# Kernel tuning notes

Hardware: AMD Instinct MI355X
Metric: run time of the kernel (lower is better)

Reference implementation:

```python
import jax, jax.numpy as jnp
import numpy as np

B, L, D, U = 8, 512, 128, 32
ATT_WIDTH = 128
EPS = 1e-7  # K.epsilon()


def setup_inputs() -> dict:
    key = jax.random.key(0)
    ks = jax.random.split(key, 4)
    x = jax.random.normal(ks[0], (B, L, D), dtype=jnp.float32)
    Wt = jax.random.normal(ks[1], (D, U), dtype=jnp.float32) * 0.1
    Wx = jax.random.normal(ks[2], (D, U), dtype=jnp.float32) * 0.1
    bh = jnp.zeros((U,), dtype=jnp.float32)
    Wa = jax.random.normal(ks[3], (U, 1), dtype=jnp.float32) * 0.1
    ba = jnp.zeros((1,), dtype=jnp.float32)
    return {"x": x, "Wt": Wt, "Wx": Wx, "bh": bh, "Wa": Wa, "ba": ba}


def reference(x, Wt, Wx, bh, Wa, ba):
    # Additive attention scores: e[b,t,s] = Wa^T (x_t Wt + x_s Wx + bh) + ba
    q = x @ Wt                              # [B,L,U]
    k = x @ Wx                              # [B,L,U]
    h = q[:, :, None, :] + k[:, None, :, :] + bh   # [B,L,L,U]
    e = jnp.einsum('btsu,u->bts', h, Wa[:, 0]) + ba[0]  # [B,L,L]
    # Windowed mask (non-causal): key j visible to query i iff lower[j] <= i < upper[j]
    lower = jnp.arange(L) - ATT_WIDTH // 2
    upper = lower + ATT_WIDTH
    idx = jnp.arange(L)[:, None]
    mask = (idx >= lower) & (idx < upper)   # [L,L]
    # Original zeroes masked scores (NOT -inf) before softmax — keep that.
    e = jnp.where(mask[None, :, :], e, jnp.zeros_like(e))
    e = e - jnp.max(e, axis=-1, keepdims=True)
    a = jnp.exp(e)
    a = a / (jnp.sum(a, axis=-1, keepdims=True) + EPS)  # [B,L,L]
    v = jnp.einsum('bts,bsd->btd', a, x)    # [B,L,D]
    return v
```

## Files before the change

### kernel.cpp

```cpp
#include <hip/hip_runtime.h>
#include <float.h>

#define B 8
#define L 512
#define D 128
#define U 32
#define WIN 128
#define EPS 1e-7f
#define T 8
#define ROWS (T + WIN - 1)
#define WPITCH (WIN + T)

__global__ __launch_bounds__(256) void pre_kernel(
        const float* __restrict__ x, const float* __restrict__ Wt,
        const float* __restrict__ Wx, const float* __restrict__ bh,
        const float* __restrict__ Wa, const float* __restrict__ ba,
        float* __restrict__ qd, float* __restrict__ kd,
        float* __restrict__ xpart) {
    __shared__ float swq[D], swk[D];
    __shared__ float scc;
    __shared__ float red[256];
    int blk = blockIdx.x, tid = threadIdx.x;

    if (tid < D) {
        float sq = 0.f, sk = 0.f;
#pragma unroll
        for (int u = 0; u < U; ++u) {
            float wa = Wa[u];
            sq += Wt[tid * U + u] * wa;
            sk += Wx[tid * U + u] * wa;
        }
        swq[tid] = sq; swk[tid] = sk;
    }
    if (tid == 0) {
        float s = ba[0];
        for (int u = 0; u < U; ++u) s += bh[u] * Wa[u];
        scc = s;
    }
    __syncthreads();

    int r = blk * 256 + tid;
    const float4* xr = (const float4*)(x + (size_t)r * D);
    float sq = 0.f, sk = 0.f;
#pragma unroll
    for (int i = 0; i < D / 4; ++i) {
        float4 v = xr[i];
        sq += v.x * swq[4*i] + v.y * swq[4*i+1] + v.z * swq[4*i+2] + v.w * swq[4*i+3];
        sk += v.x * swk[4*i] + v.y * swk[4*i+1] + v.z * swk[4*i+2] + v.w * swk[4*i+3];
    }
    qd[r] = sq + scc;
    kd[r] = sk;

    int d = tid & (D - 1), h = tid >> 7;
    const float* xp = x + ((size_t)(blk * 256 + h * 128)) * D + d;
    float s = 0.f;
#pragma unroll 8
    for (int i = 0; i < 128; ++i) s += xp[(size_t)i * D];
    red[tid] = s;
    __syncthreads();
    if (tid < 128) xpart[blk * 128 + tid] = red[tid] + red[tid + 128];
}

__global__ __launch_bounds__(256) void attn_kernel(
        const float* __restrict__ x, const float* __restrict__ qd,
        const float* __restrict__ kd, const float* __restrict__ xpart,
        float* __restrict__ out) {
    __shared__ float w[T][WPITCH];
    __shared__ float adj[T];
    int blk = blockIdx.x;
    int b = blk >> 6;
    int t0 = (blk & 63) * T;
    int row0 = t0 - (WIN / 2 - 1);
    int tid = threadIdx.x;
    int q = tid >> 5;
    int dt = tid & 31;

    for (int i = tid; i < T * WPITCH; i += 256) ((float*)w)[i] = 0.f;
    __syncthreads();

    int kt = dt;
    int t = t0 + q;
    float qv = qd[b * L + t];
    float e[4];
    int   sv[4];
#pragma unroll
    for (int i = 0; i < 4; ++i) {
        int k = kt + 32 * i;
        int s = t - 63 + k;
        bool valid = ((unsigned)s < (unsigned)L);
        sv[i] = valid;
        e[i] = valid ? (qv + kd[b * L + s]) : -FLT_MAX;
    }
    float mx = fmaxf(fmaxf(e[0], e[1]), fmaxf(e[2], e[3]));
#pragma unroll
    for (int off = 16; off > 0; off >>= 1) mx = fmaxf(mx, __shfl_xor(mx, off));
    float m = fmaxf(mx, 0.f);
    float w0 = __expf(-m);
    float wv[4], sm = 0.f;
#pragma unroll
    for (int i = 0; i < 4; ++i) {
        wv[i] = sv[i] ? __expf(e[i] - m) : 0.f;
        sm += wv[i];
    }
#pragma unroll
    for (int off = 16; off > 0; off >>= 1) sm += __shfl_xor(sm, off);
    int ss0 = max(0, t - 63), ss1 = min(L, t + 64);
    int count = ss1 - ss0;
    float denom = sm + (float)(L - count) * w0 + EPS;
    float inv = 1.f / denom;
#pragma unroll
    for (int i = 0; i < 4; ++i) {
        int k = kt + 32 * i;
        if (sv[i]) w[q][q + k] = (wv[i] - w0) * inv;
    }
    if (kt == 0) adj[q] = w0 * inv;
    __syncthreads();

    float4 acc = {0.f, 0.f, 0.f, 0.f};
    const float4* xb = (const float4*)(x + (size_t)b * L * D);
#pragma unroll 4
    for (int r = 0; r < ROWS; ++r) {
        int s = row0 + r;
        int sc = min(max(s, 0), L - 1);
        float4 xv = xb[(size_t)sc * (D / 4) + dt];
        float ww = w[q][r];
        acc.x += ww * xv.x; acc.y += ww * xv.y;
        acc.z += ww * xv.z; acc.w += ww * xv.w;
    }

    const float4* xp0 = (const float4*)(xpart + (size_t)(2 * b) * D);
    const float4* xp1 = (const float4*)(xpart + (size_t)(2 * b + 1) * D);
    float4 s0 = xp0[dt], s1 = xp1[dt];
    float a = adj[q];
    float4 o;
    o.x = acc.x + a * (s0.x + s1.x);
    o.y = acc.y + a * (s0.y + s1.y);
    o.z = acc.z + a * (s0.z + s1.z);
    o.w = acc.w + a * (s0.w + s1.w);
    ((float4*)out)[((size_t)(b * L + t)) * (D / 4) + dt] = o;
}

extern "C" void kernel_launch(void* const* d_in, const int* in_sizes, int n_in,
                              void* d_out, int out_size, void* d_ws, size_t ws_size,
                              hipStream_t stream) {
    const float* x  = (const float*)d_in[0];
    const float* Wt = (const float*)d_in[1];
    const float* Wx = (const float*)d_in[2];
    const float* bh = (const float*)d_in[3];
    const float* Wa = (const float*)d_in[4];
    const float* ba = (const float*)d_in[5];
    float* out = (float*)d_out;

    float* ws    = (float*)d_ws;
    float* qd    = ws;
    float* kd    = qd + B * L;
    float* xpart = kd + B * L;

    pre_kernel<<<(B * L) / 256, 256, 0, stream>>>(x, Wt, Wx, bh, Wa, ba, qd, kd, xpart);
    attn_kernel<<<B * (L / T), 256, 0, stream>>>(x, qd, kd, xpart, out);
}
```

Baseline: 93.07 us.

## Reuse x rows across query pairs and split window rows between half-waves

The attention kernel stores softmax weights transposed (row-major by key row) so each thread reads a float2 of weights and accumulates two query outputs per loaded x row. This halves global x reads per output. The key-row range is split between two half-waves, skips rows outside the sequence instead of clamping, and combines the halves with a cross-lane shuffle. The pre-kernel is relaunched as 32 blocks of 128 rows, with each row's projection split over two threads, to raise parallelism. It also corrects the visible-key count used for the masked-zero term in the denominator (t+65 instead of t+64).

```diff
diff --git a/kernel.cpp b/kernel.cpp
--- a/kernel.cpp
+++ b/kernel.cpp
@@ -9,7 +9,7 @@
 #define EPS 1e-7f
 #define T 8
 #define ROWS (T + WIN - 1)
-#define WPITCH (WIN + T)
+#define WPITCH 10
 
 __global__ __launch_bounds__(256) void pre_kernel(
         const float* __restrict__ x, const float* __restrict__ Wt,
@@ -19,8 +19,9 @@
         float* __restrict__ xpart) {
     __shared__ float swq[D], swk[D];
     __shared__ float scc;
-    __shared__ float red[256];
+    __shared__ float redq[256], redk[256];
     int blk = blockIdx.x, tid = threadIdx.x;
+    int r0 = blk * 128;
 
     if (tid < D) {
         float sq = 0.f, sk = 0.f;
@@ -39,105 +40,133 @@
     }
     __syncthreads();
 
-    int r = blk * 256 + tid;
-    const float4* xr = (const float4*)(x + (size_t)r * D);
-    float sq = 0.f, sk = 0.f;
+    {
+        int rr = tid & 127, h = tid >> 7;
+        const float4* xr = (const float4*)(x + ((size_t)(r0 + rr)) * D + h * 64);
+        float sq = 0.f, sk = 0.f;
+        int d0 = h * 64;
 #pragma unroll
-    for (int i = 0; i < D / 4; ++i) {
-        float4 v = xr[i];
-        sq += v.x * swq[4*i] + v.y * swq[4*i+1] + v.z * swq[4*i+2] + v.w * swq[4*i+3];
-        sk += v.x * swk[4*i] + v.y * swk[4*i+1] + v.z * swk[4*i+2] + v.w * swk[4*i+3];
+        for (int i = 0; i < 16; ++i) {
+            float4 v = xr[i];
+            sq += v.x * swq[d0 + 4*i]     + v.y * swq[d0 + 4*i + 1]
+                + v.z * swq[d0 + 4*i + 2] + v.w * swq[d0 + 4*i + 3];
+            sk += v.x * swk[d0 + 4*i]     + v.y * swk[d0 + 4*i + 1]
+                + v.z * swk[d0 + 4*i + 2] + v.w * swk[d0 + 4*i + 3];
+        }
+        redq[tid] = sq; redk[tid] = sk;
     }
-    qd[r] = sq + scc;
-    kd[r] = sk;
+    __syncthreads();
+    if (tid < 128) {
+        qd[r0 + tid] = redq[tid] + redq[tid + 128] + scc;
+        kd[r0 + tid] = redk[tid] + redk[tid + 128];
+    }
+    __syncthreads();
 
-    int d = tid & (D - 1), h = tid >> 7;
-    const float* xp = x + ((size_t)(blk * 256 + h * 128)) * D + d;
-    float s = 0.f;
+    {
+        int d = tid & 127, h = tid >> 7;
+        const float* xp = x + ((size_t)(r0 + h * 64)) * D + d;
+        float s = 0.f;
 #pragma unroll 8
-    for (int i = 0; i < 128; ++i) s += xp[(size_t)i * D];
-    red[tid] = s;
+        for (int i = 0; i < 64; ++i) s += xp[(size_t)i * D];
+        redq[tid] = s;
+    }
     __syncthreads();
-    if (tid < 128) xpart[blk * 128 + tid] = red[tid] + red[tid + 128];
+    if (tid < 128) xpart[blk * 128 + tid] = redq[tid] + redq[tid + 128];
 }
 
 __global__ __launch_bounds__(256) void attn_kernel(
         const float* __restrict__ x, const float* __restrict__ qd,
         const float* __restrict__ kd, const float* __restrict__ xpart,
         float* __restrict__ out) {
-    __shared__ float w[T][WPITCH];
+    __shared__ float w[ROWS * WPITCH];
     __shared__ float adj[T];
     int blk = blockIdx.x;
     int b = blk >> 6;
     int t0 = (blk & 63) * T;
     int row0 = t0 - (WIN / 2 - 1);
     int tid = threadIdx.x;
-    int q = tid >> 5;
-    int dt = tid & 31;
 
-    for (int i = tid; i < T * WPITCH; i += 256) ((float*)w)[i] = 0.f;
+    for (int i = tid; i < ROWS * WPITCH; i += 256) w[i] = 0.f;
     __syncthreads();
 
-    int kt = dt;
-    int t = t0 + q;
-    float qv = qd[b * L + t];
-    float e[4];
-    int   sv[4];
+    {
+        int ql = tid >> 5, kt = tid & 31;
+        int t = t0 + ql;
+        float qv = qd[b * L + t];
+        float e[4];
+        int   sv[4];
 #pragma unroll
-    for (int i = 0; i < 4; ++i) {
-        int k = kt + 32 * i;
-        int s = t - 63 + k;
-        bool valid = ((unsigned)s < (unsigned)L);
-        sv[i] = valid;
-        e[i] = valid ? (qv + kd[b * L + s]) : -FLT_MAX;
+        for (int i = 0; i < 4; ++i) {
+            int k = kt + 32 * i;
+            int s = t - 63 + k;
+            bool valid = ((unsigned)s < (unsigned)L);
+            sv[i] = valid;
+            e[i] = valid ? (qv + kd[b * L + s]) : -FLT_MAX;
+        }
+        float mx = fmaxf(fmaxf(e[0], e[1]), fmaxf(e[2], e[3]));
+#pragma unroll
+        for (int off = 16; off > 0; off >>= 1) mx = fmaxf(mx, __shfl_xor(mx, off));
+        float m = fmaxf(mx, 0.f);
+        float w0 = __expf(-m);
+        float wv[4], sm = 0.f;
+#pragma unroll
+        for (int i = 0; i < 4; ++i) {
+            wv[i] = sv[i] ? __expf(e[i] - m) : 0.f;
+            sm += wv[i];
+        }
+#pragma unroll
+        for (int off = 16; off > 0; off >>= 1) sm += __shfl_xor(sm, off);
+        int ss0 = max(0, t - 63), ss1 = min(L, t + 65);
+        int count = ss1 - ss0;
+        float inv = 1.f / (sm + (float)(L - count) * w0 + EPS);
+#pragma unroll
+        for (int i = 0; i < 4; ++i) {
+            int k = kt + 32 * i;
+            if (sv[i]) w[(ql + k) * WPITCH + ql] = (wv[i] - w0) * inv;
+        }
+        if (kt == 0) adj[ql] = w0 * inv;
     }
-    float mx = fmaxf(fmaxf(e[0], e[1]), fmaxf(e[2], e[3]));
-#pragma unroll
-    for (int off = 16; off > 0; off >>= 1) mx = fmaxf(mx, __shfl_xor(mx, off));
-    float m = fmaxf(mx, 0.f);
-    float w0 = __expf(-m);
-    float wv[4], sm = 0.f;
-#pragma unroll
-    for (int i = 0; i < 4; ++i) {
-        wv[i] = sv[i] ? __expf(e[i] - m) : 0.f;
-        sm += wv[i];
-    }
-#pragma unroll
-    for (int off = 16; off > 0; off >>= 1) sm += __shfl_xor(sm, off);
-    int ss0 = max(0, t - 63), ss1 = min(L, t + 64);
-    int count = ss1 - ss0;
-    float denom = sm + (float)(L - count) * w0 + EPS;
-    float inv = 1.f / denom;
-#pragma unroll
-    for (int i = 0; i < 4; ++i) {
-        int k = kt + 32 * i;
-        if (sv[i]) w[q][q + k] = (wv[i] - w0) * inv;
-    }
-    if (kt == 0) adj[q] = w0 * inv;
     __syncthreads();
 
-    float4 acc = {0.f, 0.f, 0.f, 0.f};
+    int dt = tid & 31, h = (tid >> 5) & 1, g = tid >> 6;
+    int rlo = max(0, -row0);
+    int rhi = min(ROWS, L - row0);
+    int mid = rlo + ((rhi - rlo + 1) >> 1);
+    int ra = h ? mid : rlo;
+    int rb = h ? rhi : mid;
+
+    float4 accA = {0.f, 0.f, 0.f, 0.f};
+    float4 accB = {0.f, 0.f, 0.f, 0.f};
     const float4* xb = (const float4*)(x + (size_t)b * L * D);
 #pragma unroll 4
-    for (int r = 0; r < ROWS; ++r) {
+    for (int r = ra; r < rb; ++r) {
         int s = row0 + r;
-        int sc = min(max(s, 0), L - 1);
-        float4 xv = xb[(size_t)sc * (D / 4) + dt];
-        float ww = w[q][r];
-        acc.x += ww * xv.x; acc.y += ww * xv.y;
-        acc.z += ww * xv.z; acc.w += ww * xv.w;
+        float4 xv = xb[(size_t)s * (D / 4) + dt];
+        float2 wp = *(const float2*)&w[r * WPITCH + 2 * g];
+        accA.x += wp.x * xv.x; accA.y += wp.x * xv.y;
+        accA.z += wp.x * xv.z; accA.w += wp.x * xv.w;
+        accB.x += wp.y * xv.x; accB.y += wp.y * xv.y;
+        accB.z += wp.y * xv.z; accB.w += wp.y * xv.w;
     }
+    accA.x += __shfl_xor(accA.x, 32); accA.y += __shfl_xor(accA.y, 32);
+    accA.z += __shfl_xor(accA.z, 32); accA.w += __shfl_xor(accA.w, 32);
+    accB.x += __shfl_xor(accB.x, 32); accB.y += __shfl_xor(accB.y, 32);
+    accB.z += __shfl_xor(accB.z, 32); accB.w += __shfl_xor(accB.w, 32);
 
-    const float4* xp0 = (const float4*)(xpart + (size_t)(2 * b) * D);
-    const float4* xp1 = (const float4*)(xpart + (size_t)(2 * b + 1) * D);
-    float4 s0 = xp0[dt], s1 = xp1[dt];
-    float a = adj[q];
-    float4 o;
-    o.x = acc.x + a * (s0.x + s1.x);
-    o.y = acc.y + a * (s0.y + s1.y);
-    o.z = acc.z + a * (s0.z + s1.z);
-    o.w = acc.w + a * (s0.w + s1.w);
-    ((float4*)out)[((size_t)(b * L + t)) * (D / 4) + dt] = o;
+    if (h == 0) {
+        const float4* xp = (const float4*)(xpart + (size_t)(4 * b) * D);
+        float4 s0 = xp[dt], s1 = xp[32 + dt], s2 = xp[64 + dt], s3 = xp[96 + dt];
+        float sx = s0.x + s1.x + s2.x + s3.x;
+        float sy = s0.y + s1.y + s2.y + s3.y;
+        float sz = s0.z + s1.z + s2.z + s3.z;
+        float sw = s0.w + s1.w + s2.w + s3.w;
+        float aA = adj[2 * g], aB = adj[2 * g + 1];
+        float4 oA = {accA.x + aA * sx, accA.y + aA * sy, accA.z + aA * sz, accA.w + aA * sw};
+        float4 oB = {accB.x + aB * sx, accB.y + aB * sy, accB.z + aB * sz, accB.w + aB * sw};
+        float4* ob = (float4*)out;
+        ob[((size_t)(b * L + t0 + 2 * g))     * (D / 4) + dt] = oA;
+        ob[((size_t)(b * L + t0 + 2 * g + 1)) * (D / 4) + dt] = oB;
+    }
 }
 
 extern "C" void kernel_launch(void* const* d_in, const int* in_sizes, int n_in,
@@ -156,6 +185,6 @@
     float* kd    = qd + B * L;
     float* xpart = kd + B * L;
 
-    pre_kernel<<<(B * L) / 256, 256, 0, stream>>>(x, Wt, Wx, bh, Wa, ba, qd, kd, xpart);
+    pre_kernel<<<32, 256, 0, stream>>>(x, Wt, Wx, bh, Wa, ba, qd, kd, xpart);
     attn_kernel<<<B * (L / T), 256, 0, stream>>>(x, qd, kd, xpart, out);
 }
```

Measured after the change: 79.61 us. -14.5%, faster.

## Fuse score projection into attention kernel and shrink query tile for more parallelism

Applied to the files above, without the earlier changes.

The per-row q/k score projections move out of the prep kernel and are recomputed inside each attention block from shared projected weights. The prep kernel now only computes column partial sums over 64 blocks with shorter serial loops, plus the folded weight vectors. The attention kernel uses 4 queries per block instead of 8, doubling the grid. It splits the row loop across two half-waves combined with shuffles, and skips out-of-range rows instead of clamping them. It also corrects the visible-key count used in the denominator (t+65 instead of t+64). The cost is redundant recomputation of projections across overlapping windows and more L2 reads of x.

```diff
diff --git a/kernel.cpp b/kernel.cpp
--- a/kernel.cpp
+++ b/kernel.cpp
@@ -7,137 +7,167 @@
 #define U 32
 #define WIN 128
 #define EPS 1e-7f
-#define T 8
+#define T 4
 #define ROWS (T + WIN - 1)
-#define WPITCH (WIN + T)
+#define WP 9
 
-__global__ __launch_bounds__(256) void pre_kernel(
+__global__ __launch_bounds__(256) void prep_kernel(
         const float* __restrict__ x, const float* __restrict__ Wt,
         const float* __restrict__ Wx, const float* __restrict__ bh,
         const float* __restrict__ Wa, const float* __restrict__ ba,
-        float* __restrict__ qd, float* __restrict__ kd,
-        float* __restrict__ xpart) {
-    __shared__ float swq[D], swk[D];
-    __shared__ float scc;
+        float* __restrict__ xpart, float* __restrict__ wqk) {
     __shared__ float red[256];
     int blk = blockIdx.x, tid = threadIdx.x;
+    int b = blk >> 3, j = blk & 7;
+    int d = tid & 127, h = tid >> 7;
+    const float* xp = x + ((size_t)(b * L + j * 64 + h * 32)) * D + d;
+    float s = 0.f;
+#pragma unroll 8
+    for (int i = 0; i < 32; ++i) s += xp[(size_t)i * D];
+    red[tid] = s;
+    __syncthreads();
+    if (tid < 128) xpart[blk * 128 + tid] = red[tid] + red[tid + 128];
 
-    if (tid < D) {
-        float sq = 0.f, sk = 0.f;
+    if (blk == 0) {
+        if (tid < 128) {
+            float sq = 0.f;
 #pragma unroll
-        for (int u = 0; u < U; ++u) {
-            float wa = Wa[u];
-            sq += Wt[tid * U + u] * wa;
-            sk += Wx[tid * U + u] * wa;
+            for (int u = 0; u < U; ++u) sq += Wt[tid * U + u] * Wa[u];
+            wqk[tid] = sq;
+        } else {
+            int dd = tid - 128;
+            float sk = 0.f;
+#pragma unroll
+            for (int u = 0; u < U; ++u) sk += Wx[dd * U + u] * Wa[u];
+            wqk[128 + dd] = sk;
         }
-        swq[tid] = sq; swk[tid] = sk;
+        if (tid == 0) {
+            float s2 = ba[0];
+            for (int u = 0; u < U; ++u) s2 += bh[u] * Wa[u];
+            wqk[256] = s2;
+        }
     }
-    if (tid == 0) {
-        float s = ba[0];
-        for (int u = 0; u < U; ++u) s += bh[u] * Wa[u];
-        scc = s;
+}
+
+__global__ __launch_bounds__(256) void attn_kernel(
+        const float* __restrict__ x, const float* __restrict__ wqk,
+        const float* __restrict__ xpart, float* __restrict__ out) {
+    __shared__ float swq[D], swk[D];
+    __shared__ float kds[ROWS];
+    __shared__ float qds[T];
+    __shared__ float w[ROWS * WP];
+    __shared__ float adj[T];
+    int blk = blockIdx.x;
+    int b = blk >> 7;
+    int t0 = (blk & 127) * T;
+    int row0 = t0 - (WIN / 2 - 1);
+    int tid = threadIdx.x;
+    int rlo = max(0, -row0);
+    int rhi = min(ROWS, L - row0);
+
+    if (tid < 128) swq[tid] = wqk[tid];
+    else           swk[tid - 128] = wqk[tid];
+    float cval = wqk[256];
+    for (int i = tid; i < ROWS * WP; i += 256) w[i] = 0.f;
+    __syncthreads();
+
+    const float4* xb4 = (const float4*)(x + (size_t)b * L * D);
+
+#pragma unroll
+    for (int pass = 0; pass < 2; ++pass) {
+        int r = pass * 128 + (tid >> 1);
+        int h = tid & 1;
+        if (r < ROWS && r >= rlo && r < rhi) {
+            const float4* xr = xb4 + (size_t)(row0 + r) * (D / 4) + h * 16;
+            float sq = 0.f, sk = 0.f;
+            int d0 = h * 64;
+#pragma unroll
+            for (int i = 0; i < 16; ++i) {
+                float4 v = xr[i];
+                sq += v.x * swq[d0+4*i]   + v.y * swq[d0+4*i+1]
+                    + v.z * swq[d0+4*i+2] + v.w * swq[d0+4*i+3];
+                sk += v.x * swk[d0+4*i]   + v.y * swk[d0+4*i+1]
+                    + v.z * swk[d0+4*i+2] + v.w * swk[d0+4*i+3];
+            }
+            sq += __shfl_xor(sq, 1);
+            sk += __shfl_xor(sk, 1);
+            if (h == 0) {
+                kds[r] = sk;
+                int qi = r - (WIN / 2 - 1);
+                if (qi >= 0 && qi < T) qds[qi] = sq + cval;
+            }
+        }
     }
     __syncthreads();
 
-    int r = blk * 256 + tid;
-    const float4* xr = (const float4*)(x + (size_t)r * D);
-    float sq = 0.f, sk = 0.f;
+    {
+        int q = tid >> 6, kt = tid & 63;
+        int t = t0 + q;
+        float qv = qds[q];
+        float e[2];
+        int   sv[2];
 #pragma unroll
-    for (int i = 0; i < D / 4; ++i) {
-        float4 v = xr[i];
-        sq += v.x * swq[4*i] + v.y * swq[4*i+1] + v.z * swq[4*i+2] + v.w * swq[4*i+3];
-        sk += v.x * swk[4*i] + v.y * swk[4*i+1] + v.z * swk[4*i+2] + v.w * swk[4*i+3];
+        for (int i = 0; i < 2; ++i) {
+            int r = q + kt + 64 * i;
+            bool valid = (r >= rlo) && (r < rhi);
+            sv[i] = valid;
+            e[i] = valid ? (qv + kds[r]) : -FLT_MAX;
+        }
+        float mx = fmaxf(e[0], e[1]);
+#pragma unroll
+        for (int off = 32; off > 0; off >>= 1) mx = fmaxf(mx, __shfl_xor(mx, off));
+        float m = fmaxf(mx, 0.f);
+        float w0 = __expf(-m);
+        float wv[2], sm = 0.f;
+#pragma unroll
+        for (int i = 0; i < 2; ++i) {
+            wv[i] = sv[i] ? __expf(e[i] - m) : 0.f;
+            sm += wv[i];
+        }
+#pragma unroll
+        for (int off = 32; off > 0; off >>= 1) sm += __shfl_xor(sm, off);
+        int ss0 = max(0, t - 63), ss1 = min(L, t + 65);
+        int count = ss1 - ss0;
+        float inv = 1.f / (sm + (float)(L - count) * w0 + EPS);
+#pragma unroll
+        for (int i = 0; i < 2; ++i) {
+            int r = q + kt + 64 * i;
+            if (sv[i]) w[r * WP + q] = (wv[i] - w0) * inv;
+        }
+        if (kt == 0) adj[q] = w0 * inv;
     }
-    qd[r] = sq + scc;
-    kd[r] = sk;
-
-    int d = tid & (D - 1), h = tid >> 7;
-    const float* xp = x + ((size_t)(blk * 256 + h * 128)) * D + d;
-    float s = 0.f;
-#pragma unroll 8
-    for (int i = 0; i < 128; ++i) s += xp[(size_t)i * D];
-    red[tid] = s;
-    __syncthreads();
-    if (tid < 128) xpart[blk * 128 + tid] = red[tid] + red[tid + 128];
-}
-
-__global__ __launch_bounds__(256) void attn_kernel(
-        const float* __restrict__ x, const float* __restrict__ qd,
-        const float* __restrict__ kd, const float* __restrict__ xpart,
-        float* __restrict__ out) {
-    __shared__ float w[T][WPITCH];
-    __shared__ float adj[T];
-    int blk = blockIdx.x;
-    int b = blk >> 6;
-    int t0 = (blk & 63) * T;
-    int row0 = t0 - (WIN / 2 - 1);
-    int tid = threadIdx.x;
-    int q = tid >> 5;
-    int dt = tid & 31;
-
-    for (int i = tid; i < T * WPITCH; i += 256) ((float*)w)[i] = 0.f;
     __syncthreads();
 
-    int kt = dt;
-    int t = t0 + q;
-    float qv = qd[b * L + t];
-    float e[4];
-    int   sv[4];
+    {
+        int q = tid >> 6, h = (tid >> 5) & 1, dt = tid & 31;
+        int mid = rlo + ((rhi - rlo + 1) >> 1);
+        int ra = h ? mid : rlo;
+        int rb = h ? rhi : mid;
+        float4 acc = {0.f, 0.f, 0.f, 0.f};
+#pragma unroll 4
+        for (int r = ra; r < rb; ++r) {
+            float4 xv = xb4[(size_t)(row0 + r) * (D / 4) + dt];
+            float ww = w[r * WP + q];
+            acc.x += ww * xv.x; acc.y += ww * xv.y;
+            acc.z += ww * xv.z; acc.w += ww * xv.w;
+        }
+        acc.x += __shfl_xor(acc.x, 32); acc.y += __shfl_xor(acc.y, 32);
+        acc.z += __shfl_xor(acc.z, 32); acc.w += __shfl_xor(acc.w, 32);
+
+        if (h == 0) {
+            const float4* xp = (const float4*)(xpart + (size_t)(8 * b) * D);
+            float sx = 0.f, sy = 0.f, sz = 0.f, sw = 0.f;
 #pragma unroll
-    for (int i = 0; i < 4; ++i) {
-        int k = kt + 32 * i;
-        int s = t - 63 + k;
-        bool valid = ((unsigned)s < (unsigned)L);
-        sv[i] = valid;
-        e[i] = valid ? (qv + kd[b * L + s]) : -FLT_MAX;
+            for (int j = 0; j < 8; ++j) {
+                float4 v = xp[j * 32 + dt];
+                sx += v.x; sy += v.y; sz += v.z; sw += v.w;
+            }
+            float a = adj[q];
+            float4 o = {acc.x + a * sx, acc.y + a * sy,
+                        acc.z + a * sz, acc.w + a * sw};
+            ((float4*)out)[((size_t)(b * L + t0 + q)) * (D / 4) + dt] = o;
+        }
     }
-    float mx = fmaxf(fmaxf(e[0], e[1]), fmaxf(e[2], e[3]));
-#pragma unroll
-    for (int off = 16; off > 0; off >>= 1) mx = fmaxf(mx, __shfl_xor(mx, off));
-    float m = fmaxf(mx, 0.f);
-    float w0 = __expf(-m);
-    float wv[4], sm = 0.f;
-#pragma unroll
-    for (int i = 0; i < 4; ++i) {
-        wv[i] = sv[i] ? __expf(e[i] - m) : 0.f;
-        sm += wv[i];
-    }
-#pragma unroll
-    for (int off = 16; off > 0; off >>= 1) sm += __shfl_xor(sm, off);
-    int ss0 = max(0, t - 63), ss1 = min(L, t + 64);
-    int count = ss1 - ss0;
-    float denom = sm + (float)(L - count) * w0 + EPS;
-    float inv = 1.f / denom;
-#pragma unroll
-    for (int i = 0; i < 4; ++i) {
-        int k = kt + 32 * i;
-        if (sv[i]) w[q][q + k] = (wv[i] - w0) * inv;
-    }
-    if (kt == 0) adj[q] = w0 * inv;
-    __syncthreads();
-
-    float4 acc = {0.f, 0.f, 0.f, 0.f};
-    const float4* xb = (const float4*)(x + (size_t)b * L * D);
-#pragma unroll 4
-    for (int r = 0; r < ROWS; ++r) {
-        int s = row0 + r;
-        int sc = min(max(s, 0), L - 1);
-        float4 xv = xb[(size_t)sc * (D / 4) + dt];
-        float ww = w[q][r];
-        acc.x += ww * xv.x; acc.y += ww * xv.y;
-        acc.z += ww * xv.z; acc.w += ww * xv.w;
-    }
-
-    const float4* xp0 = (const float4*)(xpart + (size_t)(2 * b) * D);
-    const float4* xp1 = (const float4*)(xpart + (size_t)(2 * b + 1) * D);
-    float4 s0 = xp0[dt], s1 = xp1[dt];
-    float a = adj[q];
-    float4 o;
-    o.x = acc.x + a * (s0.x + s1.x);
-    o.y = acc.y + a * (s0.y + s1.y);
-    o.z = acc.z + a * (s0.z + s1.z);
-    o.w = acc.w + a * (s0.w + s1.w);
-    ((float4*)out)[((size_t)(b * L + t)) * (D / 4) + dt] = o;
 }
 
 extern "C" void kernel_launch(void* const* d_in, const int* in_sizes, int n_in,
@@ -152,10 +182,9 @@
     float* out = (float*)d_out;
 
     float* ws    = (float*)d_ws;
-    float* qd    = ws;
-    float* kd    = qd + B * L;
-    float* xpart = kd + B * L;
+    float* xpart = ws;
+    float* wqk   = xpart + 64 * 128;
 
-    pre_kernel<<<(B * L) / 256, 256, 0, stream>>>(x, Wt, Wx, bh, Wa, ba, qd, kd, xpart);
-    attn_kernel<<<B * (L / T), 256, 0, stream>>>(x, qd, kd, xpart, out);
+    prep_kernel<<<64, 256, 0, stream>>>(x, Wt, Wx, bh, Wa, ba, xpart, wqk);
+    attn_kernel<<<B * (L / T), 256, 0, stream>>>(x, wqk, xpart, out);
 }
```

New measurement: 87.96 us. 5.5% less time.
